# Kernel tuning notes

Hardware: AMD Instinct MI355X
Metric: run time of the kernel (lower is better)

The kernel has to match this reference:

```python
import jax, jax.numpy as jnp
import numpy as np

TWO_PI = 2.0 * np.pi
MIN_W = 1e-3
MIN_H = 1e-3
MIN_D = 1e-3
DERIV_SHIFT = float(np.log(np.e - 1.0))  # softplus(x+shift)=1 at x=0


def setup_inputs() -> dict:
    key = jax.random.key(0)
    k0, k1, k2, k3 = jax.random.split(key, 4)
    B, C, H, K, Dh = 131072, 64, 256, 32, 8
    theta = jax.random.uniform(k0, (B, Dh), dtype=jnp.float32) * (TWO_PI * 0.999)
    x_conditioner = jax.random.normal(k1, (B, C), dtype=jnp.float32)
    W1 = jax.random.normal(k2, (C, H), dtype=jnp.float32) / np.sqrt(C)
    b1 = jnp.zeros((H,), jnp.float32)
    W2 = jax.random.normal(k3, (H, 3 * K * Dh), dtype=jnp.float32) / np.sqrt(H)
    b2 = jnp.zeros((3 * K * Dh,), jnp.float32)
    eta = jnp.ones((1,), jnp.float32)
    return dict(theta=theta, x_conditioner=x_conditioner, W1=W1, b1=b1, W2=W2, b2=b2, eta=eta)


def _gather(knots, idx):
    # knots: (..., K'), idx: (...) -> (...)
    return jnp.take_along_axis(knots, idx[..., None], axis=-1)[..., 0]


def _circular_rq_spline_fwd(inputs, uw, uh, ud):
    # inputs: (B, Dh) in [0, 2pi); uw/uh/ud: (B, Dh, K)
    K = uw.shape[-1]
    # circular derivatives: pad with first element so d[0] == d[K]
    ud = jnp.concatenate([ud, ud[..., :1]], axis=-1)  # (B, Dh, K+1)
    derivatives = MIN_D + jax.nn.softplus(ud)

    widths = MIN_W + (1.0 - MIN_W * K) * jax.nn.softmax(uw, axis=-1)
    cumwidths = jnp.cumsum(widths, axis=-1)
    cumwidths = jnp.pad(cumwidths, [(0, 0)] * (cumwidths.ndim - 1) + [(1, 0)])
    cumwidths = TWO_PI * cumwidths
    cumwidths = cumwidths.at[..., 0].set(0.0).at[..., -1].set(TWO_PI)
    widths = cumwidths[..., 1:] - cumwidths[..., :-1]

    heights = MIN_H + (1.0 - MIN_H * K) * jax.nn.softmax(uh, axis=-1)
    cumheights = jnp.cumsum(heights, axis=-1)
    cumheights = jnp.pad(cumheights, [(0, 0)] * (cumheights.ndim - 1) + [(1, 0)])
    cumheights = TWO_PI * cumheights
    cumheights = cumheights.at[..., 0].set(0.0).at[..., -1].set(TWO_PI)
    heights = cumheights[..., 1:] - cumheights[..., :-1]

    delta = heights / widths  # (B, Dh, K)

    # bin search (nflows-style searchsorted)
    idx = jnp.sum(inputs[..., None] >= cumwidths, axis=-1) - 1
    idx = jnp.clip(idx, 0, K - 1)

    in_cumw = _gather(cumwidths, idx)
    in_w = _gather(widths, idx)
    in_cumh = _gather(cumheights, idx)
    in_h = _gather(heights, idx)
    in_delta = _gather(delta, idx)
    in_d = _gather(derivatives, idx)
    in_d1 = _gather(derivatives[..., 1:], idx)

    t = (inputs - in_cumw) / in_w
    t1mt = t * (1.0 - t)
    numerator = in_h * (in_delta * t * t + in_d * t1mt)
    denominator = in_delta + (in_d + in_d1 - 2.0 * in_delta) * t1mt
    outputs = in_cumh + numerator / denominator

    deriv_num = in_delta * in_delta * (in_d1 * t * t + 2.0 * in_delta * t1mt + in_d * (1.0 - t) ** 2)
    logabsdet = jnp.log(deriv_num) - 2.0 * jnp.log(denominator)
    return outputs, logabsdet


def reference(theta, x_conditioner, W1, b1, W2, b2, eta):
    B, Dh = theta.shape
    K = W2.shape[-1] // (3 * Dh)
    h = jax.nn.relu(x_conditioner @ W1 + b1)
    params = (h @ W2 + b2) * eta[0]
    params = params.reshape(B, Dh, 3 * K)
    uw, uh, ud = jnp.split(params, 3, axis=-1)
    ud = ud + DERIV_SHIFT
    return _circular_rq_spline_fwd(theta, uw, uh, ud)
```

## Files before the change

### kernel.cpp

```cpp
#include <hip/hip_runtime.h>
#include <hip/hip_bf16.h>
#include <math.h>

#define B_TOTAL   131072
#define C_IN      64
#define H_DIM     256
#define K_KNOTS   32
#define DH        8
#define P_DIM     768
#define R_ROWS    32
#define NTHREADS  512

#define TWO_PI_F       6.2831853071795864769f
#define MIN_WF         1e-3f
#define MIN_HF         1e-3f
#define MIN_DF         1e-3f
#define DERIV_SHIFT_F  0.54132485461292f

typedef __attribute__((ext_vector_type(8))) short bf16x8;
typedef __attribute__((ext_vector_type(4))) float f32x4;

#define SXH_BYTE  0
#define SXL_BYTE  4096
#define SHH_BYTE  8192
#define SHL_BYTE  24576
#define SP_FLOAT  (40960 / 4)
#define LDS_BYTES 140800

#define W2P_ELEMS 196608
#define W1P_ELEMS 16384

__device__ __forceinline__ short f2bf(float x) {
    __hip_bfloat16 h = __float2bfloat16(x);
    return *reinterpret_cast<short*>(&h);
}
__device__ __forceinline__ float bf2f(short s) {
    unsigned u = ((unsigned)(unsigned short)s) << 16;
    return __uint_as_float(u);
}

__device__ __forceinline__ float softplus_f(float x) {
    return (x > 15.f) ? x : log1pf(__expf(x));
}

__global__ __launch_bounds__(256)
void pack_weights(const float* __restrict__ W1, const float* __restrict__ W2,
                  short* __restrict__ W1p_hi, short* __restrict__ W1p_lo,
                  short* __restrict__ W2p_hi, short* __restrict__ W2p_lo)
{
    const int idx = blockIdx.x * 256 + threadIdx.x;
    if (idx < W2P_ELEMS) {
        const int j  = idx & 7;
        const int l  = (idx >> 3) & 63;
        const int c  = idx >> 9;
        const int kc = c & 7;
        const int nt = c >> 3;
        const int k  = kc * 32 + (l >> 4) * 8 + j;
        const int n  = nt * 16 + (l & 15);
        const float wv = W2[k * P_DIM + n];
        const short hi = f2bf(wv);
        W2p_hi[idx] = hi;
        W2p_lo[idx] = f2bf(wv - bf2f(hi));
    } else {
        const int i2 = idx - W2P_ELEMS;
        if (i2 < W1P_ELEMS) {
            const int j  = i2 & 7;
            const int l  = (i2 >> 3) & 63;
            const int c  = i2 >> 9;
            const int kc = c & 1;
            const int nt = c >> 1;
            const int k  = kc * 32 + (l >> 4) * 8 + j;
            const int n  = nt * 16 + (l & 15);
            const float wv = W1[k * H_DIM + n];
            const short hi = f2bf(wv);
            W1p_hi[i2] = hi;
            W1p_lo[i2] = f2bf(wv - bf2f(hi));
        }
    }
}

__global__ __launch_bounds__(NTHREADS, 2)
void spline_mfma(const float* __restrict__ theta,
                 const float* __restrict__ X,
                 const short* __restrict__ W1p_hi,
                 const short* __restrict__ W1p_lo,
                 const float* __restrict__ b1,
                 const short* __restrict__ W2p_hi,
                 const short* __restrict__ W2p_lo,
                 const float* __restrict__ b2,
                 const float* __restrict__ eta,
                 float* __restrict__ out)
{
    extern __shared__ float smem[];
    char*  sXh = reinterpret_cast<char*>(smem) + SXH_BYTE;
    char*  sXl = reinterpret_cast<char*>(smem) + SXL_BYTE;
    char*  sHh = reinterpret_cast<char*>(smem) + SHH_BYTE;
    char*  sHl = reinterpret_cast<char*>(smem) + SHL_BYTE;
    float* sP  = smem + SP_FLOAT;

    const int t    = threadIdx.x;
    const int r0   = blockIdx.x * R_ROWS;
    const int lane = t & 63;
    const int w    = t >> 6;

    {
        const float4 v = reinterpret_cast<const float4*>(X + (size_t)r0 * C_IN)[t];
        const int row = t >> 4;
        const int c0  = (t & 15) * 4;
        const int slot = c0 >> 3;
        const int byte = row * 128 + (((slot ^ (row & 7)) << 4)) + ((c0 & 4) << 1);
        short4 hv, lv;
        hv.x = f2bf(v.x); lv.x = f2bf(v.x - bf2f(hv.x));
        hv.y = f2bf(v.y); lv.y = f2bf(v.y - bf2f(hv.y));
        hv.z = f2bf(v.z); lv.z = f2bf(v.z - bf2f(hv.z));
        hv.w = f2bf(v.w); lv.w = f2bf(v.w - bf2f(hv.w));
        *reinterpret_cast<short4*>(sXh + byte) = hv;
        *reinterpret_cast<short4*>(sXl + byte) = lv;
    }
    __syncthreads();

    {
        f32x4 acc[2][2] = {};
        #pragma unroll
        for (int kc = 0; kc < 2; ++kc) {
            bf16x8 ah[2], al[2];
            #pragma unroll
            for (int mt = 0; mt < 2; ++mt) {
                const int arow = mt * 16 + (lane & 15);
                const int aslot = kc * 4 + (lane >> 4);
                const int off = arow * 128 + ((aslot ^ (arow & 7)) << 4);
                ah[mt] = *reinterpret_cast<const bf16x8*>(sXh + off);
                al[mt] = *reinterpret_cast<const bf16x8*>(sXl + off);
            }
            #pragma unroll
            for (int ntl = 0; ntl < 2; ++ntl) {
                const int nt = 2 * w + ntl;
                const int boff = ((nt * 2 + kc) * 64 + lane) << 3;
                const bf16x8 bh = *reinterpret_cast<const bf16x8*>(W1p_hi + boff);
                const bf16x8 bl = *reinterpret_cast<const bf16x8*>(W1p_lo + boff);
                #pragma unroll
                for (int mt = 0; mt < 2; ++mt) {
                    acc[mt][ntl] = __builtin_amdgcn_mfma_f32_16x16x32_bf16(ah[mt], bh, acc[mt][ntl], 0, 0, 0);
                    acc[mt][ntl] = __builtin_amdgcn_mfma_f32_16x16x32_bf16(ah[mt], bl, acc[mt][ntl], 0, 0, 0);
                    acc[mt][ntl] = __builtin_amdgcn_mfma_f32_16x16x32_bf16(al[mt], bh, acc[mt][ntl], 0, 0, 0);
                }
            }
        }
        #pragma unroll
        for (int ntl = 0; ntl < 2; ++ntl) {
            const int col  = (2 * w + ntl) * 16 + (lane & 15);
            const float bias = b1[col];
            #pragma unroll
            for (int mt = 0; mt < 2; ++mt) {
                #pragma unroll
                for (int r = 0; r < 4; ++r) {
                    const int row = mt * 16 + (lane >> 4) * 4 + r;
                    float h = acc[mt][ntl][r] + bias;
                    h = h > 0.f ? h : 0.f;
                    const int byte = row * 512 + ((((col >> 3) ^ (row & 7)) << 4)) + ((col & 7) * 2);
                    const short hh = f2bf(h);
                    *reinterpret_cast<short*>(sHh + byte) = hh;
                    *reinterpret_cast<short*>(sHl + byte) = f2bf(h - bf2f(hh));
                }
            }
        }
    }
    __syncthreads();

    {
        f32x4 acc[2][6] = {};
        const int ntbase = w * 6;
        #pragma unroll
        for (int kc = 0; kc < 8; ++kc) {
            bf16x8 ah[2], al[2];
            #pragma unroll
            for (int mt = 0; mt < 2; ++mt) {
                const int arow = mt * 16 + (lane & 15);
                const int aslot = kc * 4 + (lane >> 4);
                const int off = arow * 512 + ((aslot ^ (arow & 7)) << 4);
                ah[mt] = *reinterpret_cast<const bf16x8*>(sHh + off);
                al[mt] = *reinterpret_cast<const bf16x8*>(sHl + off);
            }
            #pragma unroll
            for (int ntl = 0; ntl < 6; ++ntl) {
                const int nt = ntbase + ntl;
                const int boff = ((nt * 8 + kc) * 64 + lane) << 3;
                const bf16x8 bh = *reinterpret_cast<const bf16x8*>(W2p_hi + boff);
                const bf16x8 bl = *reinterpret_cast<const bf16x8*>(W2p_lo + boff);
                acc[0][ntl] = __builtin_amdgcn_mfma_f32_16x16x32_bf16(ah[0], bh, acc[0][ntl], 0, 0, 0);
                acc[1][ntl] = __builtin_amdgcn_mfma_f32_16x16x32_bf16(ah[1], bh, acc[1][ntl], 0, 0, 0);
                acc[0][ntl] = __builtin_amdgcn_mfma_f32_16x16x32_bf16(ah[0], bl, acc[0][ntl], 0, 0, 0);
                acc[1][ntl] = __builtin_amdgcn_mfma_f32_16x16x32_bf16(ah[1], bl, acc[1][ntl], 0, 0, 0);
                acc[0][ntl] = __builtin_amdgcn_mfma_f32_16x16x32_bf16(al[0], bh, acc[0][ntl], 0, 0, 0);
                acc[1][ntl] = __builtin_amdgcn_mfma_f32_16x16x32_bf16(al[1], bh, acc[1][ntl], 0, 0, 0);
            }
        }
        const float ev = eta[0];
        #pragma unroll
        for (int ntl = 0; ntl < 6; ++ntl) {
            const int col = (ntbase + ntl) * 16 + (lane & 15);
            const int dh  = col / 96;
            const int j   = col - dh * 96;
            const float bias = b2[col];
            #pragma unroll
            for (int mt = 0; mt < 2; ++mt) {
                #pragma unroll
                for (int r = 0; r < 4; ++r) {
                    const int row = mt * 16 + (lane >> 4) * 4 + r;
                    sP[row * 780 + dh * 97 + j] = (acc[mt][ntl][r] + bias) * ev;
                }
            }
        }
    }
    __syncthreads();

    if (t < 256) {
        const int row = t >> 3;
        const int dh  = t & 7;
        const float* p = &sP[row * 780 + dh * 97];
        const int gi = (r0 + row) * DH + dh;
        const float th = theta[gi];

        float ew[K_KNOTS], eh[K_KNOTS];
        float mw = -1e30f, mh = -1e30f;
        #pragma unroll
        for (int k = 0; k < K_KNOTS; ++k) {
            ew[k] = p[k];
            eh[k] = p[32 + k];
            mw = fmaxf(mw, ew[k]);
            mh = fmaxf(mh, eh[k]);
        }
        float sw = 0.f, sh = 0.f;
        #pragma unroll
        for (int k = 0; k < K_KNOTS; ++k) {
            ew[k] = __expf(ew[k] - mw);
            eh[k] = __expf(eh[k] - mh);
            sw += ew[k];
            sh += eh[k];
        }
        const float scw = (1.f - MIN_WF * (float)K_KNOTS) / sw;
        const float sch = (1.f - MIN_HF * (float)K_KNOTS) / sh;

        float pw = 0.f, ph = 0.f;
        float cumw = 0.f, cumh = 0.f;
        float in_cumw = 0.f, in_w = 1.f, in_cumh = 0.f, in_h = 1.f;
        int idx = 0;
        #pragma unroll
        for (int k = 0; k < K_KNOTS; ++k) {
            pw += MIN_WF + ew[k] * scw;
            ph += MIN_HF + eh[k] * sch;
            const float cumw1 = (k == K_KNOTS - 1) ? TWO_PI_F : TWO_PI_F * pw;
            const float cumh1 = (k == K_KNOTS - 1) ? TWO_PI_F : TWO_PI_F * ph;
            if (th >= cumw) {
                idx = k;
                in_cumw = cumw; in_w = cumw1 - cumw;
                in_cumh = cumh; in_h = cumh1 - cumh;
            }
            cumw = cumw1; cumh = cumh1;
        }

        const float ud0 = p[64 + idx] + DERIV_SHIFT_F;
        const int idx1 = (idx + 1) & (K_KNOTS - 1);
        const float ud1 = p[64 + idx1] + DERIV_SHIFT_F;
        const float in_d  = MIN_DF + softplus_f(ud0);
        const float in_d1 = MIN_DF + softplus_f(ud1);

        const float tt    = (th - in_cumw) / in_w;
        const float t1mt  = tt * (1.f - tt);
        const float delta = in_h / in_w;
        const float num   = in_h * (delta * tt * tt + in_d * t1mt);
        const float den   = delta + (in_d + in_d1 - 2.f * delta) * t1mt;
        const float outv  = in_cumh + num / den;
        const float omt   = 1.f - tt;
        const float dnum  = delta * delta * (in_d1 * tt * tt + 2.f * delta * t1mt + in_d * omt * omt);
        const float lad   = __logf(dnum) - 2.f * __logf(den);

        out[gi]                = outv;
        out[B_TOTAL * DH + gi] = lad;
    }
}

extern "C" void kernel_launch(void* const* d_in, const int* in_sizes, int n_in,
                              void* d_out, int out_size, void* d_ws, size_t ws_size,
                              hipStream_t stream) {
    const float* theta = (const float*)d_in[0];
    const float* X     = (const float*)d_in[1];
    const float* W1    = (const float*)d_in[2];
    const float* b1    = (const float*)d_in[3];
    const float* W2    = (const float*)d_in[4];
    const float* b2    = (const float*)d_in[5];
    const float* eta   = (const float*)d_in[6];
    float* out = (float*)d_out;

    short* W2p_hi = (short*)d_ws;
    short* W2p_lo = W2p_hi + W2P_ELEMS;
    short* W1p_hi = W2p_lo + W2P_ELEMS;
    short* W1p_lo = W1p_hi + W1P_ELEMS;

    pack_weights<<<(W2P_ELEMS + W1P_ELEMS) / 256, 256, 0, stream>>>(
        W1, W2, W1p_hi, W1p_lo, W2p_hi, W2p_lo);

    (void)hipFuncSetAttribute((const void*)spline_mfma,
                              hipFuncAttributeMaxDynamicSharedMemorySize,
                              LDS_BYTES);
    const int blocks = B_TOTAL / R_ROWS;
    spline_mfma<<<blocks, NTHREADS, LDS_BYTES, stream>>>(
        theta, X, W1p_hi, W1p_lo, b1, W2p_hi, W2p_lo, b2, eta, out);
}
```

Before: 324.3 us.

## Process 64 rows per block and alias param buffer over activation LDS

Measured after the change: 259.7 us. 19.9% less time.

```diff
diff --git a/kernel.cpp b/kernel.cpp
--- a/kernel.cpp
+++ b/kernel.cpp
@@ -8,7 +8,7 @@
 #define K_KNOTS   32
 #define DH        8
 #define P_DIM     768
-#define R_ROWS    32
+#define R_ROWS    64
 #define NTHREADS  512
 
 #define TWO_PI_F       6.2831853071795864769f
@@ -21,11 +21,10 @@
 typedef __attribute__((ext_vector_type(4))) float f32x4;
 
 #define SXH_BYTE  0
-#define SXL_BYTE  4096
-#define SHH_BYTE  8192
-#define SHL_BYTE  24576
-#define SP_FLOAT  (40960 / 4)
-#define LDS_BYTES 140800
+#define SXL_BYTE  8192
+#define SHH_BYTE  16384
+#define SHL_BYTE  49152
+#define LDS_BYTES 99840
 
 #define W2P_ELEMS 196608
 #define W1P_ELEMS 16384
@@ -79,7 +78,7 @@
     }
 }
 
-__global__ __launch_bounds__(NTHREADS, 2)
+__global__ __launch_bounds__(NTHREADS, 1)
 void spline_mfma(const float* __restrict__ theta,
                  const float* __restrict__ X,
                  const short* __restrict__ W1p_hi,
@@ -96,19 +95,21 @@
     char*  sXl = reinterpret_cast<char*>(smem) + SXL_BYTE;
     char*  sHh = reinterpret_cast<char*>(smem) + SHH_BYTE;
     char*  sHl = reinterpret_cast<char*>(smem) + SHL_BYTE;
-    float* sP  = smem + SP_FLOAT;
+    float* sP  = smem;
 
     const int t    = threadIdx.x;
     const int r0   = blockIdx.x * R_ROWS;
     const int lane = t & 63;
     const int w    = t >> 6;
 
-    {
-        const float4 v = reinterpret_cast<const float4*>(X + (size_t)r0 * C_IN)[t];
-        const int row = t >> 4;
-        const int c0  = (t & 15) * 4;
+    #pragma unroll
+    for (int i = 0; i < 2; ++i) {
+        const int idx = t + i * NTHREADS;
+        const float4 v = reinterpret_cast<const float4*>(X + (size_t)r0 * C_IN)[idx];
+        const int row = idx >> 4;
+        const int c0  = (idx & 15) * 4;
         const int slot = c0 >> 3;
-        const int byte = row * 128 + (((slot ^ (row & 7)) << 4)) + ((c0 & 4) << 1);
+        const int byte = row * 128 + ((slot ^ (row & 7)) << 4) + ((c0 & 4) << 1);
         short4 hv, lv;
         hv.x = f2bf(v.x); lv.x = f2bf(v.x - bf2f(hv.x));
         hv.y = f2bf(v.y); lv.y = f2bf(v.y - bf2f(hv.y));
@@ -120,12 +121,12 @@
     __syncthreads();
 
     {
-        f32x4 acc[2][2] = {};
+        f32x4 acc[4][2] = {};
         #pragma unroll
         for (int kc = 0; kc < 2; ++kc) {
-            bf16x8 ah[2], al[2];
-            #pragma unroll
-            for (int mt = 0; mt < 2; ++mt) {
+            bf16x8 ah[4], al[4];
+            #pragma unroll
+            for (int mt = 0; mt < 4; ++mt) {
                 const int arow = mt * 16 + (lane & 15);
                 const int aslot = kc * 4 + (lane >> 4);
                 const int off = arow * 128 + ((aslot ^ (arow & 7)) << 4);
@@ -139,7 +140,7 @@
                 const bf16x8 bh = *reinterpret_cast<const bf16x8*>(W1p_hi + boff);
                 const bf16x8 bl = *reinterpret_cast<const bf16x8*>(W1p_lo + boff);
                 #pragma unroll
-                for (int mt = 0; mt < 2; ++mt) {
+                for (int mt = 0; mt < 4; ++mt) {
                     acc[mt][ntl] = __builtin_amdgcn_mfma_f32_16x16x32_bf16(ah[mt], bh, acc[mt][ntl], 0, 0, 0);
                     acc[mt][ntl] = __builtin_amdgcn_mfma_f32_16x16x32_bf16(ah[mt], bl, acc[mt][ntl], 0, 0, 0);
                     acc[mt][ntl] = __builtin_amdgcn_mfma_f32_16x16x32_bf16(al[mt], bh, acc[mt][ntl], 0, 0, 0);
@@ -151,7 +152,7 @@
             const int col  = (2 * w + ntl) * 16 + (lane & 15);
             const float bias = b1[col];
             #pragma unroll
-            for (int mt = 0; mt < 2; ++mt) {
+            for (int mt = 0; mt < 4; ++mt) {
                 #pragma unroll
                 for (int r = 0; r < 4; ++r) {
                     const int row = mt * 16 + (lane >> 4) * 4 + r;
@@ -167,14 +168,14 @@
     }
     __syncthreads();
 
+    f32x4 acc2[4][6] = {};
     {
-        f32x4 acc[2][6] = {};
         const int ntbase = w * 6;
         #pragma unroll
         for (int kc = 0; kc < 8; ++kc) {
-            bf16x8 ah[2], al[2];
-            #pragma unroll
-            for (int mt = 0; mt < 2; ++mt) {
+            bf16x8 ah[4], al[4];
+            #pragma unroll
+            for (int mt = 0; mt < 4; ++mt) {
                 const int arow = mt * 16 + (lane & 15);
                 const int aslot = kc * 4 + (lane >> 4);
                 const int off = arow * 512 + ((aslot ^ (arow & 7)) << 4);
@@ -187,96 +188,106 @@
                 const int boff = ((nt * 8 + kc) * 64 + lane) << 3;
                 const bf16x8 bh = *reinterpret_cast<const bf16x8*>(W2p_hi + boff);
                 const bf16x8 bl = *reinterpret_cast<const bf16x8*>(W2p_lo + boff);
-                acc[0][ntl] = __builtin_amdgcn_mfma_f32_16x16x32_bf16(ah[0], bh, acc[0][ntl], 0, 0, 0);
-                acc[1][ntl] = __builtin_amdgcn_mfma_f32_16x16x32_bf16(ah[1], bh, acc[1][ntl], 0, 0, 0);
-                acc[0][ntl] = __builtin_amdgcn_mfma_f32_16x16x32_bf16(ah[0], bl, acc[0][ntl], 0, 0, 0);
-                acc[1][ntl] = __builtin_amdgcn_mfma_f32_16x16x32_bf16(ah[1], bl, acc[1][ntl], 0, 0, 0);
-                acc[0][ntl] = __builtin_amdgcn_mfma_f32_16x16x32_bf16(al[0], bh, acc[0][ntl], 0, 0, 0);
-                acc[1][ntl] = __builtin_amdgcn_mfma_f32_16x16x32_bf16(al[1], bh, acc[1][ntl], 0, 0, 0);
-            }
-        }
-        const float ev = eta[0];
-        #pragma unroll
-        for (int ntl = 0; ntl < 6; ++ntl) {
-            const int col = (ntbase + ntl) * 16 + (lane & 15);
-            const int dh  = col / 96;
-            const int j   = col - dh * 96;
-            const float bias = b2[col];
-            #pragma unroll
-            for (int mt = 0; mt < 2; ++mt) {
                 #pragma unroll
-                for (int r = 0; r < 4; ++r) {
-                    const int row = mt * 16 + (lane >> 4) * 4 + r;
-                    sP[row * 780 + dh * 97 + j] = (acc[mt][ntl][r] + bias) * ev;
-                }
-            }
-        }
-    }
+                for (int mt = 0; mt < 4; ++mt) {
+                    acc2[mt][ntl] = __builtin_amdgcn_mfma_f32_16x16x32_bf16(ah[mt], bh, acc2[mt][ntl], 0, 0, 0);
+                    acc2[mt][ntl] = __builtin_amdgcn_mfma_f32_16x16x32_bf16(ah[mt], bl, acc2[mt][ntl], 0, 0, 0);
+                    acc2[mt][ntl] = __builtin_amdgcn_mfma_f32_16x16x32_bf16(al[mt], bh, acc2[mt][ntl], 0, 0, 0);
+                }
+            }
+        }
+    }
+    const float ev = eta[0];
     __syncthreads();
 
-    if (t < 256) {
-        const int row = t >> 3;
-        const int dh  = t & 7;
-        const float* p = &sP[row * 780 + dh * 97];
-        const int gi = (r0 + row) * DH + dh;
-        const float th = theta[gi];
-
-        float ew[K_KNOTS], eh[K_KNOTS];
-        float mw = -1e30f, mh = -1e30f;
-        #pragma unroll
-        for (int k = 0; k < K_KNOTS; ++k) {
-            ew[k] = p[k];
-            eh[k] = p[32 + k];
-            mw = fmaxf(mw, ew[k]);
-            mh = fmaxf(mh, eh[k]);
-        }
-        float sw = 0.f, sh = 0.f;
-        #pragma unroll
-        for (int k = 0; k < K_KNOTS; ++k) {
-            ew[k] = __expf(ew[k] - mw);
-            eh[k] = __expf(eh[k] - mh);
-            sw += ew[k];
-            sh += eh[k];
-        }
-        const float scw = (1.f - MIN_WF * (float)K_KNOTS) / sw;
-        const float sch = (1.f - MIN_HF * (float)K_KNOTS) / sh;
-
-        float pw = 0.f, ph = 0.f;
-        float cumw = 0.f, cumh = 0.f;
-        float in_cumw = 0.f, in_w = 1.f, in_cumh = 0.f, in_h = 1.f;
-        int idx = 0;
-        #pragma unroll
-        for (int k = 0; k < K_KNOTS; ++k) {
-            pw += MIN_WF + ew[k] * scw;
-            ph += MIN_HF + eh[k] * sch;
-            const float cumw1 = (k == K_KNOTS - 1) ? TWO_PI_F : TWO_PI_F * pw;
-            const float cumh1 = (k == K_KNOTS - 1) ? TWO_PI_F : TWO_PI_F * ph;
-            if (th >= cumw) {
-                idx = k;
-                in_cumw = cumw; in_w = cumw1 - cumw;
-                in_cumh = cumh; in_h = cumh1 - cumh;
-            }
-            cumw = cumw1; cumh = cumh1;
-        }
-
-        const float ud0 = p[64 + idx] + DERIV_SHIFT_F;
-        const int idx1 = (idx + 1) & (K_KNOTS - 1);
-        const float ud1 = p[64 + idx1] + DERIV_SHIFT_F;
-        const float in_d  = MIN_DF + softplus_f(ud0);
-        const float in_d1 = MIN_DF + softplus_f(ud1);
-
-        const float tt    = (th - in_cumw) / in_w;
-        const float t1mt  = tt * (1.f - tt);
-        const float delta = in_h / in_w;
-        const float num   = in_h * (delta * tt * tt + in_d * t1mt);
-        const float den   = delta + (in_d + in_d1 - 2.f * delta) * t1mt;
-        const float outv  = in_cumh + num / den;
-        const float omt   = 1.f - tt;
-        const float dnum  = delta * delta * (in_d1 * tt * tt + 2.f * delta * t1mt + in_d * omt * omt);
-        const float lad   = __logf(dnum) - 2.f * __logf(den);
-
-        out[gi]                = outv;
-        out[B_TOTAL * DH + gi] = lad;
+    #pragma unroll
+    for (int hp = 0; hp < 2; ++hp) {
+        {
+            const int ntbase = w * 6;
+            #pragma unroll
+            for (int ntl = 0; ntl < 6; ++ntl) {
+                const int col = (ntbase + ntl) * 16 + (lane & 15);
+                const int dh  = col / 96;
+                const int j   = col - dh * 96;
+                const float bias = b2[col];
+                #pragma unroll
+                for (int mtl = 0; mtl < 2; ++mtl) {
+                    const int mt = hp * 2 + mtl;
+                    #pragma unroll
+                    for (int r = 0; r < 4; ++r) {
+                        const int rowl = mtl * 16 + (lane >> 4) * 4 + r;
+                        sP[rowl * 780 + dh * 97 + j] = (acc2[mt][ntl][r] + bias) * ev;
+                    }
+                }
+            }
+        }
+        __syncthreads();
+
+        if (t < 256) {
+            const int rowl = t >> 3;
+            const int dh   = t & 7;
+            const float* p = &sP[rowl * 780 + dh * 97];
+            const int gi = (r0 + hp * 32 + rowl) * DH + dh;
+            const float th = theta[gi];
+
+            float ew[K_KNOTS], eh[K_KNOTS];
+            float mw = -1e30f, mh = -1e30f;
+            #pragma unroll
+            for (int k = 0; k < K_KNOTS; ++k) {
+                ew[k] = p[k];
+                eh[k] = p[32 + k];
+                mw = fmaxf(mw, ew[k]);
+                mh = fmaxf(mh, eh[k]);
+            }
+            float sw = 0.f, sh = 0.f;
+            #pragma unroll
+            for (int k = 0; k < K_KNOTS; ++k) {
+                ew[k] = __expf(ew[k] - mw);
+                eh[k] = __expf(eh[k] - mh);
+                sw += ew[k];
+                sh += eh[k];
+            }
+            const float scw = (1.f - MIN_WF * (float)K_KNOTS) / sw;
+            const float sch = (1.f - MIN_HF * (float)K_KNOTS) / sh;
+
+            float pw = 0.f, ph = 0.f;
+            float cumw = 0.f, cumh = 0.f;
+            float in_cumw = 0.f, in_w = 1.f, in_cumh = 0.f, in_h = 1.f;
+            int idx = 0;
+            #pragma unroll
+            for (int k = 0; k < K_KNOTS; ++k) {
+                pw += MIN_WF + ew[k] * scw;
+                ph += MIN_HF + eh[k] * sch;
+                const float cumw1 = (k == K_KNOTS - 1) ? TWO_PI_F : TWO_PI_F * pw;
+                const float cumh1 = (k == K_KNOTS - 1) ? TWO_PI_F : TWO_PI_F * ph;
+                if (th >= cumw) {
+                    idx = k;
+                    in_cumw = cumw; in_w = cumw1 - cumw;
+                    in_cumh = cumh; in_h = cumh1 - cumh;
+                }
+                cumw = cumw1; cumh = cumh1;
+            }
+
+            const float ud0 = p[64 + idx] + DERIV_SHIFT_F;
+            const int idx1 = (idx + 1) & (K_KNOTS - 1);
+            const float ud1 = p[64 + idx1] + DERIV_SHIFT_F;
+            const float in_d  = MIN_DF + softplus_f(ud0);
+            const float in_d1 = MIN_DF + softplus_f(ud1);
+
+            const float tt    = (th - in_cumw) / in_w;
+            const float t1mt  = tt * (1.f - tt);
+            const float delta = in_h / in_w;
+            const float num   = in_h * (delta * tt * tt + in_d * t1mt);
+            const float den   = delta + (in_d + in_d1 - 2.f * delta) * t1mt;
+            const float outv  = in_cumh + num / den;
+            const float omt   = 1.f - tt;
+            const float dnum  = delta * delta * (in_d1 * tt * tt + 2.f * delta * t1mt + in_d * omt * omt);
+            const float lad   = __logf(dnum) - 2.f * __logf(den);
+
+            out[gi]                = outv;
+            out[B_TOTAL * DH + gi] = lad;
+        }
+        __syncthreads();
     }
 }
 
```
